# Optimization experiments

Measured on AMD Instinct MI355X. Metric: run time of the kernel, lower is better.

Reference implementation:

```python
import jax, jax.numpy as jnp
import numpy as np

BATCH = 8
IN_FEATURES = 4096
OUT_FEATURES = 16384


def setup_inputs() -> dict:
    key = jax.random.key(0)
    k1, k2, k3 = jax.random.split(key, 3)
    # activations, fp16 (w4a16 path)
    x = jax.random.normal(k1, (BATCH, IN_FEATURES), dtype=jnp.float16)
    # packed int4 weights: each element holds two signed 4-bit values
    # (low nibble = even column 2k, high nibble = odd column 2k+1)
    weight = jax.random.randint(k2, (OUT_FEATURES, IN_FEATURES // 2), 0, 256, dtype=jnp.int32)
    # per-output-channel symmetric scales (small positive values)
    weight_scales = (jax.random.uniform(k3, (OUT_FEATURES,), dtype=jnp.float16) * jnp.float16(0.01)
                     + jnp.float16(0.001))
    return {"x": x, "weight": weight, "weight_scales": weight_scales}


def _dequant_i4(weight, scales):
    """Unpack two signed int4 per byte and apply per-row scales.
    weight: [out, in//2] int32 (byte values 0..255); scales: [out] fp16.
    Returns [out, in] in scales.dtype.
    """
    low = weight & 0xF
    high = (weight >> 4) & 0xF
    # sign-extend 4-bit two's complement (the torch module stores signed int4;
    # mask 0x88 XOR in the kernel is the equivalent sign-bit flip)
    low = jnp.where(low >= 8, low - 16, low)
    high = jnp.where(high >= 8, high - 16, high)
    w = jnp.stack([low, high], axis=-1).reshape(weight.shape[0], -1)  # [out, in]
    return w.astype(scales.dtype) * scales[:, None]


def reference(x, weight, weight_scales):
    W = _dequant_i4(weight, weight_scales)           # [out, in] fp16
    return jnp.matmul(x, W.T)                         # [batch, out] fp16
```

## Files before the change

### kernel.cpp

```cpp
#include <hip/hip_runtime.h>
#include <stdint.h>

#define BATCH 8
#define K_DIM 4096
#define N_DIM 16384
#define KH (K_DIM / 2)
#define NPAIR (K_DIM / 2)
#define BLOCK 512
#define ROWS_PER_WAVE 4
#define ROWS_PER_BLOCK 32
#define ITERS (KH / 4 / 64)

typedef _Float16 h2 __attribute__((ext_vector_type(2)));
typedef int i4 __attribute__((ext_vector_type(4)));

__device__ __forceinline__ h2 as_h2(uint32_t u) { return __builtin_bit_cast(h2, u); }

__device__ __forceinline__ float fdot2f(h2 a, h2 b, float c) {
#if __has_builtin(__builtin_amdgcn_fdot2)
    return __builtin_amdgcn_fdot2(a, b, c, false);
#else
    return fmaf((float)a[1], (float)b[1], fmaf((float)a[0], (float)b[0], c));
#endif
}

__global__ __launch_bounds__(BLOCK, 4)
void w4a16_gemv(const float* __restrict__ x,
                const int*   __restrict__ w,
                const float* __restrict__ scales,
                float*       __restrict__ out)
{
    __shared__ uint4 xchunks[2 * NPAIR];
    const int tid = threadIdx.x;

    #pragma unroll
    for (int it = 0; it < NPAIR / BLOCK; ++it) {
        const int p = it * BLOCK + tid;
        uint32_t pk[BATCH];
        #pragma unroll
        for (int b = 0; b < BATCH; ++b) {
            const float2 v = *reinterpret_cast<const float2*>(x + (size_t)b * K_DIM + 2 * p);
            pk[b] = __builtin_bit_cast(uint32_t, __builtin_amdgcn_cvt_pkrtz(v.x, v.y));
        }
        const int c0 = 2 * p, c1 = 2 * p + 1;
        xchunks[c0 ^ ((c0 >> 3) & 7)] = make_uint4(pk[0], pk[1], pk[2], pk[3]);
        xchunks[c1 ^ ((c1 >> 3) & 7)] = make_uint4(pk[4], pk[5], pk[6], pk[7]);
    }
    __syncthreads();

    const int wave = tid >> 6;
    const int lane = tid & 63;
    const int row0 = blockIdx.x * ROWS_PER_BLOCK + wave * ROWS_PER_WAVE;

    const i4* __restrict__ wv0 = (const i4*)(w + (size_t)(row0 + 0) * KH);
    const i4* __restrict__ wv1 = (const i4*)(w + (size_t)(row0 + 1) * KH);
    const i4* __restrict__ wv2 = (const i4*)(w + (size_t)(row0 + 2) * KH);
    const i4* __restrict__ wv3 = (const i4*)(w + (size_t)(row0 + 3) * KH);

    float acc[ROWS_PER_WAVE][BATCH];
    #pragma unroll
    for (int j = 0; j < ROWS_PER_WAVE; ++j)
        #pragma unroll
        for (int b = 0; b < BATCH; ++b) acc[j][b] = 0.0f;

    const h2 neg1032 = as_h2(0xE408E408u);

    int qw[4][4];
    {
        const i4 a = __builtin_nontemporal_load(wv0 + lane);
        const i4 b = __builtin_nontemporal_load(wv1 + lane);
        const i4 c = __builtin_nontemporal_load(wv2 + lane);
        const i4 d = __builtin_nontemporal_load(wv3 + lane);
        qw[0][0] = a[0]; qw[0][1] = a[1]; qw[0][2] = a[2]; qw[0][3] = a[3];
        qw[1][0] = b[0]; qw[1][1] = b[1]; qw[1][2] = b[2]; qw[1][3] = b[3];
        qw[2][0] = c[0]; qw[2][1] = c[1]; qw[2][2] = c[2]; qw[2][3] = c[3];
        qw[3][0] = d[0]; qw[3][1] = d[1]; qw[3][2] = d[2]; qw[3][3] = d[3];
    }

    auto compute = [&](int t) {
        const int u = (t << 6) + lane;
        const int cbase = u << 3;
        const int xork = u & 7;
        #pragma unroll
        for (int m = 0; m < 4; ++m) {
            const uint4 xa = xchunks[cbase + ((2 * m)     ^ xork)];
            const uint4 xb = xchunks[cbase + ((2 * m + 1) ^ xork)];
            #pragma unroll
            for (int j = 0; j < ROWS_PER_WAVE; ++j) {
                const uint32_t bv = (uint32_t)qw[j][m];
                const uint32_t tt = (bv & 0xFu) | ((bv << 12) & 0x000F0000u);
                const h2 w2 = as_h2(tt ^ 0x64086408u) + neg1032;
                acc[j][0] = fdot2f(w2, as_h2(xa.x), acc[j][0]);
                acc[j][1] = fdot2f(w2, as_h2(xa.y), acc[j][1]);
                acc[j][2] = fdot2f(w2, as_h2(xa.z), acc[j][2]);
                acc[j][3] = fdot2f(w2, as_h2(xa.w), acc[j][3]);
                acc[j][4] = fdot2f(w2, as_h2(xb.x), acc[j][4]);
                acc[j][5] = fdot2f(w2, as_h2(xb.y), acc[j][5]);
                acc[j][6] = fdot2f(w2, as_h2(xb.z), acc[j][6]);
                acc[j][7] = fdot2f(w2, as_h2(xb.w), acc[j][7]);
            }
        }
    };

    #pragma unroll 1
    for (int t = 0; t < ITERS - 1; ++t) {
        const int un = ((t + 1) << 6) + lane;
        const i4 a = __builtin_nontemporal_load(wv0 + un);
        const i4 b = __builtin_nontemporal_load(wv1 + un);
        const i4 c = __builtin_nontemporal_load(wv2 + un);
        const i4 d = __builtin_nontemporal_load(wv3 + un);
        compute(t);
        qw[0][0] = a[0]; qw[0][1] = a[1]; qw[0][2] = a[2]; qw[0][3] = a[3];
        qw[1][0] = b[0]; qw[1][1] = b[1]; qw[1][2] = b[2]; qw[1][3] = b[3];
        qw[2][0] = c[0]; qw[2][1] = c[1]; qw[2][2] = c[2]; qw[2][3] = c[3];
        qw[3][0] = d[0]; qw[3][1] = d[1]; qw[3][2] = d[2]; qw[3][3] = d[3];
    }
    compute(ITERS - 1);

    float vals[32];
    #pragma unroll
    for (int j = 0; j < ROWS_PER_WAVE; ++j)
        #pragma unroll
        for (int b = 0; b < BATCH; ++b) vals[j * 8 + b] = acc[j][b];

    #pragma unroll
    for (int k = 0; k < 5; ++k) {
        const int sel = (lane >> k) & 1;
        const int n = 32 >> k;
        #pragma unroll
        for (int i = 0; i < n / 2; ++i) {
            const float a = vals[2 * i];
            const float c = vals[2 * i + 1];
            const float mine  = sel ? c : a;
            const float other = sel ? a : c;
            vals[i] = mine + __shfl_xor(other, 1 << k, 64);
        }
    }
    const float total = vals[0] + __shfl_xor(vals[0], 32, 64);

    if (lane < 32) {
        const int r = row0 + (lane >> 3);
        out[(size_t)(lane & 7) * N_DIM + r] = total * scales[r];
    }
}

extern "C" void kernel_launch(void* const* d_in, const int* in_sizes, int n_in,
                              void* d_out, int out_size, void* d_ws, size_t ws_size,
                              hipStream_t stream) {
    const float* x      = (const float*)d_in[0];
    const int*   w      = (const int*)d_in[1];
    const float* scales = (const float*)d_in[2];
    float*       out    = (float*)d_out;

    dim3 grid(N_DIM / ROWS_PER_BLOCK);
    dim3 block(BLOCK);
    hipLaunchKernelGGL(w4a16_gemv, grid, block, 0, stream, x, w, scales, out);
}
```

Baseline: 194.2 us.

## Double-buffer weight prefetch and issue first loads before x staging

Issues the first two weight tile loads before the activation-staging phase so global weight latency overlaps the x conversion and LDS writes. The main loop now alternates two register buffers, giving a prefetch distance of two iterations instead of one. The x staging loop uses float4 loads with an adjusted swizzle, and the fdot2 fallback path is removed. This doubles the live weight registers, which may raise register pressure against the launch bounds occupancy target.

```diff
diff --git a/kernel.cpp b/kernel.cpp
--- a/kernel.cpp
+++ b/kernel.cpp
@@ -17,11 +17,7 @@
 __device__ __forceinline__ h2 as_h2(uint32_t u) { return __builtin_bit_cast(h2, u); }
 
 __device__ __forceinline__ float fdot2f(h2 a, h2 b, float c) {
-#if __has_builtin(__builtin_amdgcn_fdot2)
     return __builtin_amdgcn_fdot2(a, b, c, false);
-#else
-    return fmaf((float)a[1], (float)b[1], fmaf((float)a[0], (float)b[0], c));
-#endif
 }
 
 __global__ __launch_bounds__(BLOCK, 4)
@@ -32,22 +28,6 @@
 {
     __shared__ uint4 xchunks[2 * NPAIR];
     const int tid = threadIdx.x;
-
-    #pragma unroll
-    for (int it = 0; it < NPAIR / BLOCK; ++it) {
-        const int p = it * BLOCK + tid;
-        uint32_t pk[BATCH];
-        #pragma unroll
-        for (int b = 0; b < BATCH; ++b) {
-            const float2 v = *reinterpret_cast<const float2*>(x + (size_t)b * K_DIM + 2 * p);
-            pk[b] = __builtin_bit_cast(uint32_t, __builtin_amdgcn_cvt_pkrtz(v.x, v.y));
-        }
-        const int c0 = 2 * p, c1 = 2 * p + 1;
-        xchunks[c0 ^ ((c0 >> 3) & 7)] = make_uint4(pk[0], pk[1], pk[2], pk[3]);
-        xchunks[c1 ^ ((c1 >> 3) & 7)] = make_uint4(pk[4], pk[5], pk[6], pk[7]);
-    }
-    __syncthreads();
-
     const int wave = tid >> 6;
     const int lane = tid & 63;
     const int row0 = blockIdx.x * ROWS_PER_BLOCK + wave * ROWS_PER_WAVE;
@@ -57,6 +37,42 @@
     const i4* __restrict__ wv2 = (const i4*)(w + (size_t)(row0 + 2) * KH);
     const i4* __restrict__ wv3 = (const i4*)(w + (size_t)(row0 + 3) * KH);
 
+    int qwA[4][4], qwB[4][4];
+
+    auto loadset = [&](int (&qw)[4][4], int t) {
+        const int u = (t << 6) + lane;
+        const i4 a = __builtin_nontemporal_load(wv0 + u);
+        const i4 b = __builtin_nontemporal_load(wv1 + u);
+        const i4 c = __builtin_nontemporal_load(wv2 + u);
+        const i4 d = __builtin_nontemporal_load(wv3 + u);
+        qw[0][0] = a[0]; qw[0][1] = a[1]; qw[0][2] = a[2]; qw[0][3] = a[3];
+        qw[1][0] = b[0]; qw[1][1] = b[1]; qw[1][2] = b[2]; qw[1][3] = b[3];
+        qw[2][0] = c[0]; qw[2][1] = c[1]; qw[2][2] = c[2]; qw[2][3] = c[3];
+        qw[3][0] = d[0]; qw[3][1] = d[1]; qw[3][2] = d[2]; qw[3][3] = d[3];
+    };
+
+    loadset(qwA, 0);
+    loadset(qwB, 1);
+
+    #pragma unroll
+    for (int it = 0; it < NPAIR / 2 / BLOCK; ++it) {
+        const int q = it * BLOCK + tid;
+        uint32_t pk0[BATCH], pk1[BATCH];
+        #pragma unroll
+        for (int b = 0; b < BATCH; ++b) {
+            const float4 v = *reinterpret_cast<const float4*>(x + (size_t)b * K_DIM + 4 * q);
+            pk0[b] = __builtin_bit_cast(uint32_t, __builtin_amdgcn_cvt_pkrtz(v.x, v.y));
+            pk1[b] = __builtin_bit_cast(uint32_t, __builtin_amdgcn_cvt_pkrtz(v.z, v.w));
+        }
+        const int c0 = 4 * q;
+        const int s = (q >> 1) & 7;
+        xchunks[(c0 + 0) ^ s] = make_uint4(pk0[0], pk0[1], pk0[2], pk0[3]);
+        xchunks[(c0 + 1) ^ s] = make_uint4(pk0[4], pk0[5], pk0[6], pk0[7]);
+        xchunks[(c0 + 2) ^ s] = make_uint4(pk1[0], pk1[1], pk1[2], pk1[3]);
+        xchunks[(c0 + 3) ^ s] = make_uint4(pk1[4], pk1[5], pk1[6], pk1[7]);
+    }
+    __syncthreads();
+
     float acc[ROWS_PER_WAVE][BATCH];
     #pragma unroll
     for (int j = 0; j < ROWS_PER_WAVE; ++j)
@@ -65,19 +81,7 @@
 
     const h2 neg1032 = as_h2(0xE408E408u);
 
-    int qw[4][4];
-    {
-        const i4 a = __builtin_nontemporal_load(wv0 + lane);
-        const i4 b = __builtin_nontemporal_load(wv1 + lane);
-        const i4 c = __builtin_nontemporal_load(wv2 + lane);
-        const i4 d = __builtin_nontemporal_load(wv3 + lane);
-        qw[0][0] = a[0]; qw[0][1] = a[1]; qw[0][2] = a[2]; qw[0][3] = a[3];
-        qw[1][0] = b[0]; qw[1][1] = b[1]; qw[1][2] = b[2]; qw[1][3] = b[3];
-        qw[2][0] = c[0]; qw[2][1] = c[1]; qw[2][2] = c[2]; qw[2][3] = c[3];
-        qw[3][0] = d[0]; qw[3][1] = d[1]; qw[3][2] = d[2]; qw[3][3] = d[3];
-    }
-
-    auto compute = [&](int t) {
+    auto compute = [&](int (&qw)[4][4], int t) {
         const int u = (t << 6) + lane;
         const int cbase = u << 3;
         const int xork = u & 7;
@@ -103,19 +107,14 @@
     };
 
     #pragma unroll 1
-    for (int t = 0; t < ITERS - 1; ++t) {
-        const int un = ((t + 1) << 6) + lane;
-        const i4 a = __builtin_nontemporal_load(wv0 + un);
-        const i4 b = __builtin_nontemporal_load(wv1 + un);
-        const i4 c = __builtin_nontemporal_load(wv2 + un);
-        const i4 d = __builtin_nontemporal_load(wv3 + un);
-        compute(t);
-        qw[0][0] = a[0]; qw[0][1] = a[1]; qw[0][2] = a[2]; qw[0][3] = a[3];
-        qw[1][0] = b[0]; qw[1][1] = b[1]; qw[1][2] = b[2]; qw[1][3] = b[3];
-        qw[2][0] = c[0]; qw[2][1] = c[1]; qw[2][2] = c[2]; qw[2][3] = c[3];
-        qw[3][0] = d[0]; qw[3][1] = d[1]; qw[3][2] = d[2]; qw[3][3] = d[3];
+    for (int t = 0; t < ITERS - 2; t += 2) {
+        compute(qwA, t);
+        loadset(qwA, t + 2);
+        compute(qwB, t + 1);
+        loadset(qwB, t + 3);
     }
-    compute(ITERS - 1);
+    compute(qwA, ITERS - 2);
+    compute(qwB, ITERS - 1);
 
     float vals[32];
     #pragma unroll
```

Measured after the change: 197.2 us. Within noise of the previous version (+1.6%).
